# Performance work log

Hardware: AMD Instinct MI355X
Metric: run time of the kernel (lower is better)

The kernel has to match this reference:

```python
import jax, jax.numpy as jnp
import numpy as np

B, T, D = 32, 1024, 512

def _xavier(key, shape):
    fan_in, fan_out = shape[1], shape[0]
    bound = float(np.sqrt(6.0 / (fan_in + fan_out)))
    return jax.random.uniform(key, shape, jnp.float32, -bound, bound)

def setup_inputs() -> dict:
    key = jax.random.key(0)
    ks = jax.random.split(key, 10)
    lin_bound = float(1.0 / np.sqrt(D))
    def lin(kw, kb):
        W = jax.random.uniform(kw, (D, D), jnp.float32, -lin_bound, lin_bound)
        b = jax.random.uniform(kb, (D,), jnp.float32, -lin_bound, lin_bound)
        return W, b
    Wk_w, Wk_b = lin(ks[0], ks[1])
    Wv_w, Wv_b = lin(ks[2], ks[3])
    Wq_w, Wq_b = lin(ks[4], ks[5])
    Wo_w, Wo_b = lin(ks[6], ks[7])
    w = _xavier(ks[8], (T, T))
    x = jax.random.normal(ks[9], (B, T, D), jnp.float32)
    return {"x": x, "Wk_w": Wk_w, "Wk_b": Wk_b, "Wv_w": Wv_w, "Wv_b": Wv_b,
            "Wq_w": Wq_w, "Wq_b": Wq_b, "w": w, "Wo_w": Wo_w, "Wo_b": Wo_b}

def reference(x, Wk_w, Wk_b, Wv_w, Wv_b, Wq_w, Wq_b, w, Wo_w, Wo_b):
    # K, V, Q: [B, T, D]  (torch Linear: x @ W.T + b)
    K = jnp.einsum('btd,ed->bte', x, Wk_w) + Wk_b
    V = jnp.einsum('btd,ed->bte', x, Wv_w) + Wv_b
    # exp_w: [T, T], row-wise max-stabilized position bias
    exp_w = jnp.exp(w - jnp.max(w, axis=-1, keepdims=True))
    # Faithful to original: max over dim=0 (batch dim) of K
    exp_K = jnp.exp(K - jnp.max(K, axis=0, keepdims=True))  # [B, T, D]
    num = jnp.einsum('ts,bsd->btd', exp_w, exp_K * V)
    den = jnp.einsum('ts,bsd->btd', exp_w, exp_K)
    Yt = num / den
    Q = jnp.einsum('btd,ed->bte', x, Wq_w) + Wq_b
    Yt = jax.nn.sigmoid(Q) * Yt
    out = jnp.einsum('btd,ed->bte', Yt, Wo_w) + Wo_b
    return out
```

## Files before the change

kernel.cpp:

```cpp
#include <hip/hip_runtime.h>
#include <stdint.h>

typedef unsigned short u16;
typedef __attribute__((ext_vector_type(4))) float f32x4;
typedef __attribute__((ext_vector_type(8))) __bf16 bf16x8;

__device__ __forceinline__ float b2f(u16 u) {
  union { unsigned int i; float f; } v; v.i = ((unsigned int)u) << 16; return v.f;
}
__device__ __forceinline__ u16 f2b(float f) {
  union { float f; unsigned int i; } v; v.f = f;
  unsigned int x = v.i;
  return (u16)((x + 0x7fffu + ((x >> 16) & 1u)) >> 16);
}

__device__ __forceinline__ void async_ld16(const u16* g, u16* l) {
  __builtin_amdgcn_global_load_lds((const __attribute__((address_space(1))) void*)g,
                                   (__attribute__((address_space(3))) void*)l, 16, 0, 0);
}

__global__ void detect_kernel(const u16* __restrict__ x, int* __restrict__ flag)
{
  const int tid = threadIdx.x;
  int found = 0;
  for (int i = tid; i < 32768; i += 256) {
    u16 u = x[i];
    if ((u & 0x7F80u) == 0x7F80u) found = 1;
  }
  unsigned long long m = __ballot(found != 0);
  __shared__ int sf[4];
  if ((tid & 63) == 0) sf[tid >> 6] = (m != 0ULL) ? 1 : 0;
  __syncthreads();
  if (tid == 0) flag[0] = (sf[0] | sf[1] | sf[2] | sf[3]);
}

__global__ __launch_bounds__(256)
void conv_kernel(const void* __restrict__ in, u16* __restrict__ out, long n,
                 const int* __restrict__ flag)
{
  const long i = ((long)blockIdx.x * 256 + threadIdx.x) * 8;
  if (i >= n) return;
  if (flag[0]) {
    const float* p = (const float*)in + i;
    u16 o[8];
#pragma unroll
    for (int j = 0; j < 8; j++) o[j] = f2b(p[j]);
    *(uint4*)(out + i) = *(const uint4*)o;
  } else {
    *(uint4*)(out + i) = *(const uint4*)((const u16*)in + i);
  }
}

__global__ __launch_bounds__(256)
void conv4_kernel(const void* __restrict__ i0, const void* __restrict__ i1,
                  const void* __restrict__ i2, const void* __restrict__ i3,
                  u16* __restrict__ o0, u16* __restrict__ o1,
                  u16* __restrict__ o2, u16* __restrict__ o3,
                  const int* __restrict__ flag)
{
  const int sel = blockIdx.x >> 7;
  const int blk = blockIdx.x & 127;
  const void* in = (sel == 0) ? i0 : (sel == 1) ? i1 : (sel == 2) ? i2 : i3;
  u16* out = (sel == 0) ? o0 : (sel == 1) ? o1 : (sel == 2) ? o2 : o3;
  const long i = ((long)blk * 256 + threadIdx.x) * 8;
  if (flag[0]) {
    const float* p = (const float*)in + i;
    u16 o[8];
#pragma unroll
    for (int j = 0; j < 8; j++) o[j] = f2b(p[j]);
    *(uint4*)(out + i) = *(const uint4*)o;
  } else {
    *(uint4*)(out + i) = *(const uint4*)((const u16*)in + i);
  }
}

#define BM 128
#define BN 128
#define BK 32

template<int EPI>
__global__ __launch_bounds__(256)
void gemm_bt(const u16* __restrict__ A, const u16* __restrict__ B,
             const void* __restrict__ bias, void* __restrict__ Cv,
             const int* __restrict__ flag,
             int M, int N, int K, long strideC)
{
  __shared__ __align__(16) u16 sA[2][BM * BK];
  __shared__ __align__(16) u16 sB[2][BN * BK];

  const int tid  = threadIdx.x;
  const int lane = tid & 63;
  const int wv   = tid >> 6;
  const int fl = flag[0];
  u16* Cb16 = (u16*)Cv;

  int bx = blockIdx.x, by = blockIdx.y;
  {
    const int nx = gridDim.x, ny = gridDim.y;
    if ((nx & 7) == 0) {
      const int d   = bx + nx * by;
      const int xcd = d & 7;
      const int s   = d >> 3;
      const int q   = s / ny;
      bx = xcd * (nx >> 3) + q;
      by = s - q * ny;
    }
  }
  const int m0 = bx * BM;
  const int n0 = by * BN;

  const int ldRow = wv * 32;
  const int lr = lane >> 2;
  const int lc = lane & 3;
  const int scol = (lc ^ ((lr >> 1) & 3)) * 8;
  const u16* gA = A + (long)(m0 + ldRow + lr) * K + scol;
  const u16* gB = B + (long)(n0 + ldRow + lr) * K + scol;
  const int off0 = (ldRow + lr) * BK + lc * 8;
  const int off1 = (ldRow + 16 + lr) * BK + lc * 8;

  f32x4 acc[4][4];
#pragma unroll
  for (int i = 0; i < 4; i++)
#pragma unroll
    for (int j = 0; j < 4; j++) acc[i][j] = (f32x4)0.0f;

  const int waveM = (wv >> 1) * 64;
  const int waveN = (wv & 1) * 64;
  const int quad  = lane >> 4;
  const int ll    = lane & 15;
  const int rs    = (quad ^ ((ll >> 1) & 3)) * 8;

  async_ld16(gA,          sA[0] + off0);
  async_ld16(gA + 16 * K, sA[0] + off1);
  async_ld16(gB,          sB[0] + off0);
  async_ld16(gB + 16 * K, sB[0] + off1);
  gA += BK; gB += BK;

  const int NT = K / BK;
  for (int t = 0; t < NT; ++t) {
    __syncthreads();
    const int cur = t & 1;
    if (t + 1 < NT) {
      u16* dA = sA[cur ^ 1];
      u16* dB = sB[cur ^ 1];
      async_ld16(gA,          dA + off0);
      async_ld16(gA + 16 * K, dA + off1);
      async_ld16(gB,          dB + off0);
      async_ld16(gB + 16 * K, dB + off1);
      gA += BK; gB += BK;
    }
    const u16* rA = sA[cur];
    const u16* rB = sB[cur];
    bf16x8 aF[4], bF[4];
#pragma unroll
    for (int i = 0; i < 4; i++) {
      aF[i] = *(const bf16x8*)(rA + (waveM + i * 16 + ll) * BK + rs);
      bF[i] = *(const bf16x8*)(rB + (waveN + i * 16 + ll) * BK + rs);
    }
#pragma unroll
    for (int i = 0; i < 4; i++)
#pragma unroll
      for (int j = 0; j < 4; j++)
        acc[i][j] = __builtin_amdgcn_mfma_f32_16x16x32_bf16(aF[i], bF[j], acc[i][j], 0, 0, 0);
  }

#pragma unroll
  for (int i = 0; i < 4; i++) {
    const int rowb = m0 + waveM + i * 16 + quad * 4;
#pragma unroll
    for (int j = 0; j < 4; j++) {
      const int col = n0 + waveN + j * 16 + ll;
      const float bv = fl ? ((const float*)bias)[col] : b2f(((const u16*)bias)[col]);
#pragma unroll
      for (int r = 0; r < 4; r++) {
        const long idx = (long)(rowb + r) * N + col;
        const float v = acc[i][j][r] + bv;
        if (EPI == 0) {
          Cb16[idx] = f2b(v);
        } else {
          const long g = strideC + idx;
          if (fl) ((float*)Cv)[g] = v;
          else    ((u16*)Cv)[g]   = f2b(v);
        }
      }
    }
  }
}

__global__ __launch_bounds__(256)
void gemm_proj3(const u16* __restrict__ A, const u16* __restrict__ Bw,
                const void* __restrict__ kb, const void* __restrict__ vb,
                const void* __restrict__ qb,
                u16* __restrict__ Kp, u16* __restrict__ Vp, u16* __restrict__ Qp,
                const int* __restrict__ flag, int M)
{
  const int KD = 512;
  __shared__ __align__(16) u16 sA[2][BM * BK];
  __shared__ __align__(16) u16 sB[2][BN * BK];

  const int tid  = threadIdx.x;
  const int lane = tid & 63;
  const int wv   = tid >> 6;
  const int fl = flag[0];

  int bx = blockIdx.x, by = blockIdx.y;
  {
    const int nx = gridDim.x, ny = gridDim.y;
    if ((nx & 7) == 0) {
      const int d   = bx + nx * by;
      const int xcd = d & 7;
      const int s   = d >> 3;
      const int q   = s / ny;
      bx = xcd * (nx >> 3) + q;
      by = s - q * ny;
    }
  }
  const int m0 = bx * BM;
  const int n0 = by * BN;

  const int ldRow = wv * 32;
  const int lr = lane >> 2;
  const int lc = lane & 3;
  const int scol = (lc ^ ((lr >> 1) & 3)) * 8;
  const u16* gA = A  + (long)(m0 + ldRow + lr) * KD + scol;
  const u16* gB = Bw + (long)(n0 + ldRow + lr) * KD + scol;
  const int off0 = (ldRow + lr) * BK + lc * 8;
  const int off1 = (ldRow + 16 + lr) * BK + lc * 8;

  f32x4 acc[4][4];
#pragma unroll
  for (int i = 0; i < 4; i++)
#pragma unroll
    for (int j = 0; j < 4; j++) acc[i][j] = (f32x4)0.0f;

  const int waveM = (wv >> 1) * 64;
  const int waveN = (wv & 1) * 64;
  const int quad  = lane >> 4;
  const int ll    = lane & 15;
  const int rs    = (quad ^ ((ll >> 1) & 3)) * 8;

  async_ld16(gA,           sA[0] + off0);
  async_ld16(gA + 16 * KD, sA[0] + off1);
  async_ld16(gB,           sB[0] + off0);
  async_ld16(gB + 16 * KD, sB[0] + off1);
  gA += BK; gB += BK;

  const int NT = KD / BK;
  for (int t = 0; t < NT; ++t) {
    __syncthreads();
    const int cur = t & 1;
    if (t + 1 < NT) {
      u16* dA = sA[cur ^ 1];
      u16* dB = sB[cur ^ 1];
      async_ld16(gA,           dA + off0);
      async_ld16(gA + 16 * KD, dA + off1);
      async_ld16(gB,           dB + off0);
      async_ld16(gB + 16 * KD, dB + off1);
      gA += BK; gB += BK;
    }
    const u16* rA = sA[cur];
    const u16* rB = sB[cur];
    bf16x8 aF[4], bF[4];
#pragma unroll
    for (int i = 0; i < 4; i++) {
      aF[i] = *(const bf16x8*)(rA + (waveM + i * 16 + ll) * BK + rs);
      bF[i] = *(const bf16x8*)(rB + (waveN + i * 16 + ll) * BK + rs);
    }
#pragma unroll
    for (int i = 0; i < 4; i++)
#pragma unroll
      for (int j = 0; j < 4; j++)
        acc[i][j] = __builtin_amdgcn_mfma_f32_16x16x32_bf16(aF[i], bF[j], acc[i][j], 0, 0, 0);
  }

#pragma unroll
  for (int i = 0; i < 4; i++) {
    const int rowb = m0 + waveM + i * 16 + quad * 4;
#pragma unroll
    for (int j = 0; j < 4; j++) {
      const int col = n0 + waveN + j * 16 + ll;
      const int sel = col >> 9;
      const int cs  = col & 511;
      const void* bp = (sel == 0) ? kb : (sel == 1) ? vb : qb;
      u16* dst = (sel == 0) ? Kp : (sel == 1) ? Vp : Qp;
      const float bv = fl ? ((const float*)bp)[cs] : b2f(((const u16*)bp)[cs]);
#pragma unroll
      for (int r = 0; r < 4; r++)
        dst[(long)(rowb + r) * 512 + cs] = f2b(acc[i][j][r] + bv);
    }
  }
}

#define AM 128
#define AN 64
#define ABK 32

__global__ __launch_bounds__(256, 2)
void gemm_aft(const u16* __restrict__ ew, const u16* __restrict__ Pt,
              const u16* __restrict__ PVt, const u16* __restrict__ Q,
              u16* __restrict__ Yt)
{
  const int T = 1024, D = 512;
  __shared__ __align__(16) u16 sA[2][AM * ABK];
  __shared__ __align__(16) u16 sB[2][AN * ABK];
  __shared__ __align__(16) u16 sC[2][AN * ABK];

  const int tid  = threadIdx.x;
  const int lane = tid & 63;
  const int wv   = tid >> 6;

  int xt = blockIdx.x, yt = blockIdx.y, zt = blockIdx.z;
  {
    const int nz = gridDim.z;
    const int d   = xt + (yt << 3) + (zt << 6);
    const int xcd = d & 7;
    const int s   = d >> 3;
    const int panel = xcd * nz + (s >> 3);
    xt = s & 7;
    yt = panel & 7;
    zt = panel >> 3;
  }
  const int b = zt;

  const u16* Ptb  = Pt  + (long)b * D * T;
  const u16* PVtb = PVt + (long)b * D * T;
  const u16* Qb   = Q   + (long)b * T * D;
  u16*       Ytb  = Yt  + (long)b * T * D;

  const int m0 = xt * AM;
  const int n0 = yt * AN;

  const int ldRow = wv * 16;
  const int lr = lane >> 2;
  const int lc = lane & 3;
  const int scol = (lc ^ ((lr >> 1) & 3)) * 8;
  const u16* gA = ew   + (long)(m0 + ldRow + lr) * T + scol;
  const u16* gB = Ptb  + (long)(n0 + ldRow + lr) * T + scol;
  const u16* gC = PVtb + (long)(n0 + ldRow + lr) * T + scol;
  const int offA0 = (ldRow + lr) * ABK + lc * 8;
  const int offA1 = (64 + ldRow + lr) * ABK + lc * 8;
  const int offB0 = (ldRow + lr) * ABK + lc * 8;

  f32x4 accN[4][2], accD[4][2];
#pragma unroll
  for (int i = 0; i < 4; i++)
#pragma unroll
    for (int j = 0; j < 2; j++) { accN[i][j] = (f32x4)0.0f; accD[i][j] = (f32x4)0.0f; }

  const int waveM = (wv >> 1) * 64;
  const int waveN = (wv & 1) * 32;
  const int quad  = lane >> 4;
  const int ll    = lane & 15;
  const int rs    = (quad ^ ((ll >> 1) & 3)) * 8;

  async_ld16(gA,          sA[0] + offA0);
  async_ld16(gA + 64 * T, sA[0] + offA1);
  async_ld16(gB,          sB[0] + offB0);
  async_ld16(gC,          sC[0] + offB0);
  gA += ABK; gB += ABK; gC += ABK;

  const int NT = T / ABK;
  for (int t = 0; t < NT; ++t) {
    __syncthreads();
    const int cur = t & 1;
    if (t + 1 < NT) {
      u16* dA = sA[cur ^ 1];
      u16* dB = sB[cur ^ 1];
      u16* dC = sC[cur ^ 1];
      async_ld16(gA,          dA + offA0);
      async_ld16(gA + 64 * T, dA + offA1);
      async_ld16(gB,          dB + offB0);
      async_ld16(gC,          dC + offB0);
      gA += ABK; gB += ABK; gC += ABK;
    }
    const u16* rA = sA[cur];
    const u16* rB = sB[cur];
    const u16* rC = sC[cur];
    bf16x8 aF[4], bF[2], cF[2];
#pragma unroll
    for (int i = 0; i < 4; i++)
      aF[i] = *(const bf16x8*)(rA + (waveM + i * 16 + ll) * ABK + rs);
#pragma unroll
    for (int j = 0; j < 2; j++) {
      bF[j] = *(const bf16x8*)(rB + (waveN + j * 16 + ll) * ABK + rs);
      cF[j] = *(const bf16x8*)(rC + (waveN + j * 16 + ll) * ABK + rs);
    }
#pragma unroll
    for (int i = 0; i < 4; i++)
#pragma unroll
      for (int j = 0; j < 2; j++) {
        accD[i][j] = __builtin_amdgcn_mfma_f32_16x16x32_bf16(aF[i], bF[j], accD[i][j], 0, 0, 0);
        accN[i][j] = __builtin_amdgcn_mfma_f32_16x16x32_bf16(aF[i], cF[j], accN[i][j], 0, 0, 0);
      }
  }

#pragma unroll
  for (int i = 0; i < 4; i++) {
    const int rowb = m0 + waveM + i * 16 + quad * 4;
#pragma unroll
    for (int j = 0; j < 2; j++) {
      const int col = n0 + waveN + j * 16 + ll;
#pragma unroll
      for (int r = 0; r < 4; r++) {
        const long idx = (long)(rowb + r) * D + col;
        const float q  = b2f(Qb[idx]);
        const float t  = __expf(-q);
        const float rc = __builtin_amdgcn_rcpf(accD[i][j][r] * (1.0f + t));
        Ytb[idx] = f2b(accN[i][j][r] * rc);
      }
    }
  }
}

__global__ __launch_bounds__(256)
void expw_kernel(const void* __restrict__ w, u16* __restrict__ ew,
                 const int* __restrict__ flag)
{
  const int fl = flag[0];
  const int t = blockIdx.x;
  const int tid = threadIdx.x;
  float v[4];
  float m = -1e30f;
#pragma unroll
  for (int i = 0; i < 4; i++) {
    const long idx = (long)t * 1024 + tid + i * 256;
    float val = fl ? ((const float*)w)[idx] : b2f(((const u16*)w)[idx]);
    v[i] = val; m = fmaxf(m, val);
  }
#pragma unroll
  for (int off = 32; off > 0; off >>= 1) m = fmaxf(m, __shfl_xor(m, off, 64));
  __shared__ float sm[4];
  if ((tid & 63) == 0) sm[tid >> 6] = m;
  __syncthreads();
  m = fmaxf(fmaxf(sm[0], sm[1]), fmaxf(sm[2], sm[3]));
  u16* orow = ew + (long)t * 1024;
#pragma unroll
  for (int i = 0; i < 4; i++) orow[tid + i * 256] = f2b(__expf(v[i] - m));
}

__global__ __launch_bounds__(256)
void kmax_kernel(const u16* __restrict__ K, u16* __restrict__ Km)
{
  const long TD = 1024L * 512;
  const long base = ((long)blockIdx.x * 256 + threadIdx.x) * 8;
  float m[8];
#pragma unroll
  for (int j = 0; j < 8; j++) m[j] = -1e30f;
  for (int b = 0; b < 32; b++) {
    uint4 u = *(const uint4*)(K + b * TD + base);
    const u16* p = (const u16*)&u;
#pragma unroll
    for (int j = 0; j < 8; j++) m[j] = fmaxf(m[j], b2f(p[j]));
  }
  u16 outv[8];
#pragma unroll
  for (int j = 0; j < 8; j++) outv[j] = f2b(m[j]);
  *(uint4*)(Km + base) = *(const uint4*)outv;
}

__global__ __launch_bounds__(256)
void pexp_kernel(const u16* __restrict__ K, const u16* __restrict__ V,
                 const u16* __restrict__ Km,
                 u16* __restrict__ Pt, u16* __restrict__ PVt)
{
  const int T = 1024, D = 512;
  const long TD = (long)T * D;
  const int s0 = blockIdx.x * 64;
  const int d0 = blockIdx.y * 64;
  const int b  = blockIdx.z;
  __shared__ u16 lp[64 * 66];
  __shared__ u16 lpv[64 * 66];
  const int tid  = threadIdx.x;
  const int srow = tid >> 3;
  const int c8   = (tid & 7) * 8;

#pragma unroll
  for (int h = 0; h < 2; h++) {
    const int s = srow + h * 32;
    const long gidx = (long)b * TD + (long)(s0 + s) * D + d0 + c8;
    uint4 ku = *(const uint4*)(K + gidx);
    uint4 vu = *(const uint4*)(V + gidx);
    uint4 mu = *(const uint4*)(Km + (long)(s0 + s) * D + d0 + c8);
    const u16* kp = (const u16*)&ku;
    const u16* vp = (const u16*)&vu;
    const u16* mp = (const u16*)&mu;
#pragma unroll
    for (int j = 0; j < 8; j++) {
      float p  = __expf(b2f(kp[j]) - b2f(mp[j]));
      float pv = p * b2f(vp[j]);
      lp[s * 66 + c8 + j]  = f2b(p);
      lpv[s * 66 + c8 + j] = f2b(pv);
    }
  }
  __syncthreads();

  const int lane = tid & 63;
  const int wv   = tid >> 6;
#pragma unroll
  for (int it = 0; it < 16; it++) {
    const int d = wv * 16 + it;
    const long oidx = (long)b * TD + (long)(d0 + d) * T + s0 + lane;
    Pt[oidx]  = lp[lane * 66 + d];
    PVt[oidx] = lpv[lane * 66 + d];
  }
}

extern "C" void kernel_launch(void* const* d_in, const int* in_sizes, int n_in,
                              void* d_out, int out_size, void* d_ws, size_t ws_size,
                              hipStream_t stream)
{
  const int B = 32, T = 1024, D = 512;
  const long TD = (long)T * D;
  const void* x    = d_in[0];
  const void* Wk_w = d_in[1];
  const void* Wk_b = d_in[2];
  const void* Wv_w = d_in[3];
  const void* Wv_b = d_in[4];
  const void* Wq_w = d_in[5];
  const void* Wq_b = d_in[6];
  const void* w    = d_in[7];
  const void* Wo_w = d_in[8];
  const void* Wo_b = d_in[9];

  char* ws = (char*)d_ws;
  const size_t MB = 1024 * 1024;
  u16* xb    = (u16*)(ws + 0);
  u16* Kbuf  = (u16*)(ws + 32 * MB);
  u16* ewb   = (u16*)(ws + 64 * MB);
  u16* kmb   = (u16*)(ws + 66 * MB);
  u16* Wpack = (u16*)(ws + 67 * MB);
  u16* Wvb   = Wpack + 512 * 512;
  u16* Wqb   = Wpack + 2 * 512 * 512;
  u16* Wob   = (u16*)(ws + 68 * MB + 512 * 1024);
  int* flag  = (int*)(ws + 69 * MB);
  u16* Ytb   = Kbuf;

  dim3 blk(256);

  detect_kernel<<<dim3(1), blk, 0, stream>>>((const u16*)x, flag);
  conv_kernel<<<dim3(8192), blk, 0, stream>>>(x, xb, (long)B * T * D, flag);
  conv4_kernel<<<dim3(512), blk, 0, stream>>>(Wk_w, Wv_w, Wq_w, Wo_w,
                                              Wpack, Wvb, Wqb, Wob, flag);
  expw_kernel<<<dim3(1024), blk, 0, stream>>>(w, ewb, flag);

  if (ws_size >= 200 * MB) {
    u16* Vb   = (u16*)(ws + 70 * MB);
    u16* Qb   = (u16*)(ws + 102 * MB);
    u16* Ptb  = (u16*)(ws + 134 * MB);
    u16* PVtb = (u16*)(ws + 166 * MB);

    gemm_proj3<<<dim3((B * T) / 128, 12), blk, 0, stream>>>(
        xb, Wpack, Wk_b, Wv_b, Wq_b, Kbuf, Vb, Qb, flag, B * T);

    kmax_kernel<<<dim3(256), blk, 0, stream>>>(Kbuf, kmb);
    pexp_kernel<<<dim3(16, 8, 32), blk, 0, stream>>>(Kbuf, Vb, kmb, Ptb, PVtb);

    gemm_aft<<<dim3(T / AM, D / AN, 32), blk, 0, stream>>>(ewb, Ptb, PVtb, Qb, Ytb);

    gemm_bt<3><<<dim3((B * T) / 128, D / 128), blk, 0, stream>>>(
        Ytb, Wob, Wo_b, d_out, flag, B * T, D, D, 0);
  } else {
    const int NB = 4, NC = B / NB;
    char* ck = ws + 70 * MB;
    const size_t cb = (size_t)NB * TD * sizeof(u16);
    u16* Vc   = (u16*)(ck);
    u16* Ptc  = (u16*)(ck + cb);
    u16* PVtc = (u16*)(ck + 2 * cb);
    u16* Qc   = (u16*)(ck + 3 * cb);
    u16* Ytc  = Vc;

    gemm_bt<0><<<dim3((B * T) / 128, D / 128), blk, 0, stream>>>(
        xb, Wpack, Wk_b, Kbuf, flag, B * T, D, D, 0);
    kmax_kernel<<<dim3(256), blk, 0, stream>>>(Kbuf, kmb);

    dim3 gP((NB * T) / 128, D / 128, 1);
    dim3 gA(T / AM, D / AN, NB);
    for (int c = 0; c < NC; c++) {
      const long off = (long)c * NB * TD;
      gemm_bt<0><<<gP, blk, 0, stream>>>(xb + off, Wvb, Wv_b, Vc, flag, NB * T, D, D, 0);
      gemm_bt<0><<<gP, blk, 0, stream>>>(xb + off, Wqb, Wq_b, Qc, flag, NB * T, D, D, 0);
      pexp_kernel<<<dim3(16, 8, NB), blk, 0, stream>>>(Kbuf + off, Vc, kmb, Ptc, PVtc);
      gemm_aft<<<gA, blk, 0, stream>>>(ewb, Ptc, PVtc, Qc, Ytc);
      gemm_bt<3><<<gP, blk, 0, stream>>>(Ytc, Wob, Wo_b, d_out, flag, NB * T, D, D, off);
    }
  }
}
```

Before: 379.6 us.

## Triple-buffer LDS tiles with partial vmcnt waits in all GEMM kernels

Moves the three GEMM kernels (generic, fused QKV projection, AFT num/den) from double- to triple-buffered shared-memory staging. Loads now run two K-tiles ahead, and the full __syncthreads is replaced by an s_waitcnt vmcnt(4) plus barrier, so only the oldest tile's loads must land before compute. This is meant to hide more global-load latency behind MFMA work. In exchange it uses 50% more LDS per block, which may reduce occupancy, and the correctness of the hand-written wait counts depends on each thread issuing exactly four loads per tile.

```diff
diff --git a/kernel.cpp b/kernel.cpp
--- a/kernel.cpp
+++ b/kernel.cpp
@@ -17,6 +17,17 @@
 __device__ __forceinline__ void async_ld16(const u16* g, u16* l) {
   __builtin_amdgcn_global_load_lds((const __attribute__((address_space(1))) void*)g,
                                    (__attribute__((address_space(3))) void*)l, 16, 0, 0);
+}
+
+__device__ __forceinline__ void pipe_wait4() {
+  asm volatile("s_waitcnt vmcnt(4)" ::: "memory");
+  __builtin_amdgcn_s_barrier();
+  asm volatile("" ::: "memory");
+}
+__device__ __forceinline__ void pipe_wait0() {
+  asm volatile("s_waitcnt vmcnt(0)" ::: "memory");
+  __builtin_amdgcn_s_barrier();
+  asm volatile("" ::: "memory");
 }
 
 __global__ void detect_kernel(const u16* __restrict__ x, int* __restrict__ flag)
@@ -85,8 +96,8 @@
              const int* __restrict__ flag,
              int M, int N, int K, long strideC)
 {
-  __shared__ __align__(16) u16 sA[2][BM * BK];
-  __shared__ __align__(16) u16 sB[2][BN * BK];
+  __shared__ __align__(16) u16 sA[3][BM * BK];
+  __shared__ __align__(16) u16 sB[3][BN * BK];
 
   const int tid  = threadIdx.x;
   const int lane = tid & 63;
@@ -135,14 +146,20 @@
   async_ld16(gB,          sB[0] + off0);
   async_ld16(gB + 16 * K, sB[0] + off1);
   gA += BK; gB += BK;
+  async_ld16(gA,          sA[1] + off0);
+  async_ld16(gA + 16 * K, sA[1] + off1);
+  async_ld16(gB,          sB[1] + off0);
+  async_ld16(gB + 16 * K, sB[1] + off1);
+  gA += BK; gB += BK;
 
   const int NT = K / BK;
+  int cur = 0;
   for (int t = 0; t < NT; ++t) {
-    __syncthreads();
-    const int cur = t & 1;
-    if (t + 1 < NT) {
-      u16* dA = sA[cur ^ 1];
-      u16* dB = sB[cur ^ 1];
+    if (t < NT - 1) pipe_wait4(); else pipe_wait0();
+    if (t + 2 < NT) {
+      int pre = cur + 2; if (pre >= 3) pre -= 3;
+      u16* dA = sA[pre];
+      u16* dB = sB[pre];
       async_ld16(gA,          dA + off0);
       async_ld16(gA + 16 * K, dA + off1);
       async_ld16(gB,          dB + off0);
@@ -162,6 +179,7 @@
 #pragma unroll
       for (int j = 0; j < 4; j++)
         acc[i][j] = __builtin_amdgcn_mfma_f32_16x16x32_bf16(aF[i], bF[j], acc[i][j], 0, 0, 0);
+    cur += 1; if (cur == 3) cur = 0;
   }
 
 #pragma unroll
@@ -195,8 +213,8 @@
                 const int* __restrict__ flag, int M)
 {
   const int KD = 512;
-  __shared__ __align__(16) u16 sA[2][BM * BK];
-  __shared__ __align__(16) u16 sB[2][BN * BK];
+  __shared__ __align__(16) u16 sA[3][BM * BK];
+  __shared__ __align__(16) u16 sB[3][BN * BK];
 
   const int tid  = threadIdx.x;
   const int lane = tid & 63;
@@ -244,14 +262,20 @@
   async_ld16(gB,           sB[0] + off0);
   async_ld16(gB + 16 * KD, sB[0] + off1);
   gA += BK; gB += BK;
+  async_ld16(gA,           sA[1] + off0);
+  async_ld16(gA + 16 * KD, sA[1] + off1);
+  async_ld16(gB,           sB[1] + off0);
+  async_ld16(gB + 16 * KD, sB[1] + off1);
+  gA += BK; gB += BK;
 
   const int NT = KD / BK;
+  int cur = 0;
   for (int t = 0; t < NT; ++t) {
-    __syncthreads();
-    const int cur = t & 1;
-    if (t + 1 < NT) {
-      u16* dA = sA[cur ^ 1];
-      u16* dB = sB[cur ^ 1];
+    if (t < NT - 1) pipe_wait4(); else pipe_wait0();
+    if (t + 2 < NT) {
+      int pre = cur + 2; if (pre >= 3) pre -= 3;
+      u16* dA = sA[pre];
+      u16* dB = sB[pre];
       async_ld16(gA,           dA + off0);
       async_ld16(gA + 16 * KD, dA + off1);
       async_ld16(gB,           dB + off0);
@@ -271,6 +295,7 @@
 #pragma unroll
       for (int j = 0; j < 4; j++)
         acc[i][j] = __builtin_amdgcn_mfma_f32_16x16x32_bf16(aF[i], bF[j], acc[i][j], 0, 0, 0);
+    cur += 1; if (cur == 3) cur = 0;
   }
 
 #pragma unroll
@@ -301,9 +326,9 @@
               u16* __restrict__ Yt)
 {
   const int T = 1024, D = 512;
-  __shared__ __align__(16) u16 sA[2][AM * ABK];
-  __shared__ __align__(16) u16 sB[2][AN * ABK];
-  __shared__ __align__(16) u16 sC[2][AN * ABK];
+  __shared__ __align__(16) u16 sA[3][AM * ABK];
+  __shared__ __align__(16) u16 sB[3][AN * ABK];
+  __shared__ __align__(16) u16 sC[3][AN * ABK];
 
   const int tid  = threadIdx.x;
   const int lane = tid & 63;
@@ -358,15 +383,21 @@
   async_ld16(gB,          sB[0] + offB0);
   async_ld16(gC,          sC[0] + offB0);
   gA += ABK; gB += ABK; gC += ABK;
+  async_ld16(gA,          sA[1] + offA0);
+  async_ld16(gA + 64 * T, sA[1] + offA1);
+  async_ld16(gB,          sB[1] + offB0);
+  async_ld16(gC,          sC[1] + offB0);
+  gA += ABK; gB += ABK; gC += ABK;
 
   const int NT = T / ABK;
+  int cur = 0;
   for (int t = 0; t < NT; ++t) {
-    __syncthreads();
-    const int cur = t & 1;
-    if (t + 1 < NT) {
-      u16* dA = sA[cur ^ 1];
-      u16* dB = sB[cur ^ 1];
-      u16* dC = sC[cur ^ 1];
+    if (t < NT - 1) pipe_wait4(); else pipe_wait0();
+    if (t + 2 < NT) {
+      int pre = cur + 2; if (pre >= 3) pre -= 3;
+      u16* dA = sA[pre];
+      u16* dB = sB[pre];
+      u16* dC = sC[pre];
       async_ld16(gA,          dA + offA0);
       async_ld16(gA + 64 * T, dA + offA1);
       async_ld16(gB,          dB + offB0);
@@ -392,6 +423,7 @@
         accD[i][j] = __builtin_amdgcn_mfma_f32_16x16x32_bf16(aF[i], bF[j], accD[i][j], 0, 0, 0);
         accN[i][j] = __builtin_amdgcn_mfma_f32_16x16x32_bf16(aF[i], cF[j], accN[i][j], 0, 0, 0);
       }
+    cur += 1; if (cur == 3) cur = 0;
   }
 
 #pragma unroll
```

New measurement: 383.0 us. No clear change (+0.9%).

## Enlarge AFT GEMM tile to 256x128 with 8 waves and interleaved prefetch

Applied to the files above, without the earlier changes.

Rewrites gemm_aft to use 512-thread blocks, each computing a 256x128 output tile with a K step of 64 split into two 32-wide sub-stages. Global-to-LDS prefetch of the next stage is interleaved between MFMA phases, with explicit barriers, waitcnt and setprio to overlap memory and compute. The XCD-aware block remapping is adjusted to the new 4x4 grid. Larger tiles cut redundant loads of exp_w and P tiles. In exchange the kernel uses more LDS and registers, which may lower occupancy, and the hand-written waitcnt sequence is fragile.

```diff
diff --git a/kernel.cpp b/kernel.cpp
--- a/kernel.cpp
+++ b/kernel.cpp
@@ -291,19 +291,15 @@
   }
 }
 
-#define AM 128
-#define AN 64
-#define ABK 32
-
-__global__ __launch_bounds__(256, 2)
+__global__ __launch_bounds__(512, 2)
 void gemm_aft(const u16* __restrict__ ew, const u16* __restrict__ Pt,
               const u16* __restrict__ PVt, const u16* __restrict__ Q,
               u16* __restrict__ Yt)
 {
   const int T = 1024, D = 512;
-  __shared__ __align__(16) u16 sA[2][AM * ABK];
-  __shared__ __align__(16) u16 sB[2][AN * ABK];
-  __shared__ __align__(16) u16 sC[2][AN * ABK];
+  __shared__ __align__(16) u16 sA[2 * 2 * 256 * 32];
+  __shared__ __align__(16) u16 sB[2 * 2 * 128 * 32];
+  __shared__ __align__(16) u16 sC[2 * 2 * 128 * 32];
 
   const int tid  = threadIdx.x;
   const int lane = tid & 63;
@@ -312,79 +308,85 @@
   int xt = blockIdx.x, yt = blockIdx.y, zt = blockIdx.z;
   {
     const int nz = gridDim.z;
-    const int d   = xt + (yt << 3) + (zt << 6);
-    const int xcd = d & 7;
-    const int s   = d >> 3;
-    const int panel = xcd * nz + (s >> 3);
-    xt = s & 7;
-    yt = panel & 7;
-    zt = panel >> 3;
+    if ((nz & 1) == 0) {
+      const int d   = xt + (yt << 2) + (zt << 4);
+      const int xcd = d & 7;
+      const int s   = d >> 3;
+      xt = s & 3;
+      const int p = xcd * (nz >> 1) + (s >> 2);
+      yt = p & 3;
+      zt = p >> 2;
+    }
   }
   const int b = zt;
-
   const u16* Ptb  = Pt  + (long)b * D * T;
   const u16* PVtb = PVt + (long)b * D * T;
   const u16* Qb   = Q   + (long)b * T * D;
   u16*       Ytb  = Yt  + (long)b * T * D;
-
-  const int m0 = xt * AM;
-  const int n0 = yt * AN;
-
-  const int ldRow = wv * 16;
-  const int lr = lane >> 2;
-  const int lc = lane & 3;
-  const int scol = (lc ^ ((lr >> 1) & 3)) * 8;
-  const u16* gA = ew   + (long)(m0 + ldRow + lr) * T + scol;
-  const u16* gB = Ptb  + (long)(n0 + ldRow + lr) * T + scol;
-  const u16* gC = PVtb + (long)(n0 + ldRow + lr) * T + scol;
-  const int offA0 = (ldRow + lr) * ABK + lc * 8;
-  const int offA1 = (64 + ldRow + lr) * ABK + lc * 8;
-  const int offB0 = (ldRow + lr) * ABK + lc * 8;
-
-  f32x4 accN[4][2], accD[4][2];
-#pragma unroll
-  for (int i = 0; i < 4; i++)
+  const int m0 = xt * 256;
+  const int n0 = yt * 128;
+
+  const int sr = tid >> 2, ss = tid & 3;
+  const int sslot = (ss ^ ((sr >> 1) & 3)) * 8;
+  const u16* gA0 = ew   + (long)(m0 + sr)       * T + sslot;
+  const u16* gA1 = ew   + (long)(m0 + 128 + sr) * T + sslot;
+  const u16* gB  = Ptb  + (long)(n0 + sr)       * T + sslot;
+  const u16* gC  = PVtb + (long)(n0 + sr)       * T + sslot;
+  const int soff = sr * 32 + ss * 8;
+
+  f32x4 accN[8][2], accD[8][2];
+#pragma unroll
+  for (int i = 0; i < 8; i++)
 #pragma unroll
     for (int j = 0; j < 2; j++) { accN[i][j] = (f32x4)0.0f; accD[i][j] = (f32x4)0.0f; }
 
-  const int waveM = (wv >> 1) * 64;
-  const int waveN = (wv & 1) * 32;
   const int quad  = lane >> 4;
   const int ll    = lane & 15;
   const int rs    = (quad ^ ((ll >> 1) & 3)) * 8;
-
-  async_ld16(gA,          sA[0] + offA0);
-  async_ld16(gA + 64 * T, sA[0] + offA1);
-  async_ld16(gB,          sB[0] + offB0);
-  async_ld16(gC,          sC[0] + offB0);
-  gA += ABK; gB += ABK; gC += ABK;
-
-  const int NT = T / ABK;
+  const int waveM = (wv >> 2) * 128;
+  const int waveN = (wv & 3) * 32;
+
+  async_ld16(gA0,      sA + soff);
+  async_ld16(gA1,      sA + 4096 + soff);
+  async_ld16(gB,       sB + soff);
+  async_ld16(gC,       sC + soff);
+  async_ld16(gA0 + 32, sA + 8192 + soff);
+  async_ld16(gA1 + 32, sA + 8192 + 4096 + soff);
+  async_ld16(gB  + 32, sB + 4096 + soff);
+  async_ld16(gC  + 32, sC + 4096 + soff);
+  asm volatile("s_waitcnt vmcnt(4)" ::: "memory");
+  __builtin_amdgcn_s_barrier();
+
+  const int NT = T / 64;
   for (int t = 0; t < NT; ++t) {
-    __syncthreads();
     const int cur = t & 1;
-    if (t + 1 < NT) {
-      u16* dA = sA[cur ^ 1];
-      u16* dB = sB[cur ^ 1];
-      u16* dC = sC[cur ^ 1];
-      async_ld16(gA,          dA + offA0);
-      async_ld16(gA + 64 * T, dA + offA1);
-      async_ld16(gB,          dB + offB0);
-      async_ld16(gC,          dC + offB0);
-      gA += ABK; gB += ABK; gC += ABK;
-    }
-    const u16* rA = sA[cur];
-    const u16* rB = sB[cur];
-    const u16* rC = sC[cur];
+    const u16* bA = sA + cur * 16384;
+    const u16* bB = sB + cur * 8192;
+    const u16* bC = sC + cur * 8192;
+    u16* nA = sA + (cur ^ 1) * 16384;
+    u16* nB = sB + (cur ^ 1) * 8192;
+    u16* nC = sC + (cur ^ 1) * 8192;
+    const int ko = (t + 1) * 64;
+    const bool st = (t + 1 < NT);
+
     bf16x8 aF[4], bF[2], cF[2];
-#pragma unroll
-    for (int i = 0; i < 4; i++)
-      aF[i] = *(const bf16x8*)(rA + (waveM + i * 16 + ll) * ABK + rs);
+
+#pragma unroll
+    for (int i = 0; i < 4; i++)
+      aF[i] = *(const bf16x8*)(bA + (waveM + i * 16 + ll) * 32 + rs);
 #pragma unroll
     for (int j = 0; j < 2; j++) {
-      bF[j] = *(const bf16x8*)(rB + (waveN + j * 16 + ll) * ABK + rs);
-      cF[j] = *(const bf16x8*)(rC + (waveN + j * 16 + ll) * ABK + rs);
-    }
+      bF[j] = *(const bf16x8*)(bB + (waveN + j * 16 + ll) * 32 + rs);
+      cF[j] = *(const bf16x8*)(bC + (waveN + j * 16 + ll) * 32 + rs);
+    }
+    if (st) {
+      async_ld16(gA0 + ko, nA + soff);
+      async_ld16(gA1 + ko, nA + 4096 + soff);
+    }
+    __builtin_amdgcn_s_barrier();
+    asm volatile("s_waitcnt lgkmcnt(0)" ::: "memory");
+    __builtin_amdgcn_sched_barrier(0);
+    __builtin_amdgcn_s_setprio(1);
 #pragma unroll
     for (int i = 0; i < 4; i++)
 #pragma unroll
@@ -392,10 +394,87 @@
         accD[i][j] = __builtin_amdgcn_mfma_f32_16x16x32_bf16(aF[i], bF[j], accD[i][j], 0, 0, 0);
         accN[i][j] = __builtin_amdgcn_mfma_f32_16x16x32_bf16(aF[i], cF[j], accN[i][j], 0, 0, 0);
       }
-  }
-
-#pragma unroll
-  for (int i = 0; i < 4; i++) {
+    __builtin_amdgcn_s_setprio(0);
+    __builtin_amdgcn_s_barrier();
+
+#pragma unroll
+    for (int i = 0; i < 4; i++)
+      aF[i] = *(const bf16x8*)(bA + (waveM + (4 + i) * 16 + ll) * 32 + rs);
+    if (st) {
+      async_ld16(gB + ko, nB + soff);
+      async_ld16(gC + ko, nC + soff);
+    }
+    __builtin_amdgcn_s_barrier();
+    asm volatile("s_waitcnt lgkmcnt(0)" ::: "memory");
+    __builtin_amdgcn_sched_barrier(0);
+    __builtin_amdgcn_s_setprio(1);
+#pragma unroll
+    for (int i = 0; i < 4; i++)
+#pragma unroll
+      for (int j = 0; j < 2; j++) {
+        accD[4 + i][j] = __builtin_amdgcn_mfma_f32_16x16x32_bf16(aF[i], bF[j], accD[4 + i][j], 0, 0, 0);
+        accN[4 + i][j] = __builtin_amdgcn_mfma_f32_16x16x32_bf16(aF[i], cF[j], accN[4 + i][j], 0, 0, 0);
+      }
+    __builtin_amdgcn_s_setprio(0);
+    if (st) asm volatile("s_waitcnt vmcnt(4)" ::: "memory");
+    else    asm volatile("s_waitcnt vmcnt(0)" ::: "memory");
+    __builtin_amdgcn_s_barrier();
+
+    const u16* bA1 = bA + 8192;
+    const u16* bB1 = bB + 4096;
+    const u16* bC1 = bC + 4096;
+#pragma unroll
+    for (int i = 0; i < 4; i++)
+      aF[i] = *(const bf16x8*)(bA1 + (waveM + i * 16 + ll) * 32 + rs);
+#pragma unroll
+    for (int j = 0; j < 2; j++) {
+      bF[j] = *(const bf16x8*)(bB1 + (waveN + j * 16 + ll) * 32 + rs);
+      cF[j] = *(const bf16x8*)(bC1 + (waveN + j * 16 + ll) * 32 + rs);
+    }
+    if (st) {
+      async_ld16(gA0 + ko + 32, nA + 8192 + soff);
+      async_ld16(gA1 + ko + 32, nA + 8192 + 4096 + soff);
+    }
+    __builtin_amdgcn_s_barrier();
+    asm volatile("s_waitcnt lgkmcnt(0)" ::: "memory");
+    __builtin_amdgcn_sched_barrier(0);
+    __builtin_amdgcn_s_setprio(1);
+#pragma unroll
+    for (int i = 0; i < 4; i++)
+#pragma unroll
+      for (int j = 0; j < 2; j++) {
+        accD[i][j] = __builtin_amdgcn_mfma_f32_16x16x32_bf16(aF[i], bF[j], accD[i][j], 0, 0, 0);
+        accN[i][j] = __builtin_amdgcn_mfma_f32_16x16x32_bf16(aF[i], cF[j], accN[i][j], 0, 0, 0);
+      }
+    __builtin_amdgcn_s_setprio(0);
+    __builtin_amdgcn_s_barrier();
+
+#pragma unroll
+    for (int i = 0; i < 4; i++)
+      aF[i] = *(const bf16x8*)(bA1 + (waveM + (4 + i) * 16 + ll) * 32 + rs);
+    if (st) {
+      async_ld16(gB + ko + 32, nB + 4096 + soff);
+      async_ld16(gC + ko + 32, nC + 4096 + soff);
+    }
+    __builtin_amdgcn_s_barrier();
+    asm volatile("s_waitcnt lgkmcnt(0)" ::: "memory");
+    __builtin_amdgcn_sched_barrier(0);
+    __builtin_amdgcn_s_setprio(1);
+#pragma unroll
+    for (int i = 0; i < 4; i++)
+#pragma unroll
+      for (int j = 0; j < 2; j++) {
+        accD[4 + i][j] = __builtin_amdgcn_mfma_f32_16x16x32_bf16(aF[i], bF[j], accD[4 + i][j], 0, 0, 0);
+        accN[4 + i][j] = __builtin_amdgcn_mfma_f32_16x16x32_bf16(aF[i], cF[j], accN[4 + i][j], 0, 0, 0);
+      }
+    __builtin_amdgcn_s_setprio(0);
+    if (st) asm volatile("s_waitcnt vmcnt(4)" ::: "memory");
+    else    asm volatile("s_waitcnt vmcnt(0)" ::: "memory");
+    __builtin_amdgcn_s_barrier();
+  }
+
+#pragma unroll
+  for (int i = 0; i < 8; i++) {
     const int rowb = m0 + waveM + i * 16 + quad * 4;
 #pragma unroll
     for (int j = 0; j < 2; j++) {
@@ -404,8 +483,8 @@
       for (int r = 0; r < 4; r++) {
         const long idx = (long)(rowb + r) * D + col;
         const float q  = b2f(Qb[idx]);
-        const float t  = __expf(-q);
-        const float rc = __builtin_amdgcn_rcpf(accD[i][j][r] * (1.0f + t));
+        const float e  = __expf(-q);
+        const float rc = __builtin_amdgcn_rcpf(accD[i][j][r] * (1.0f + e));
         Ytb[idx] = f2b(accN[i][j][r] * rc);
       }
     }
@@ -555,7 +634,7 @@
     kmax_kernel<<<dim3(256), blk, 0, stream>>>(Kbuf, kmb);
     pexp_kernel<<<dim3(16, 8, 32), blk, 0, stream>>>(Kbuf, Vb, kmb, Ptb, PVtb);
 
-    gemm_aft<<<dim3(T / AM, D / AN, 32), blk, 0, stream>>>(ewb, Ptb, PVtb, Qb, Ytb);
+    gemm_aft<<<dim3(4, 4, 32), dim3(512), 0, stream>>>(ewb, Ptb, PVtb, Qb, Ytb);
 
     gemm_bt<3><<<dim3((B * T) / 128, D / 128), blk, 0, stream>>>(
         Ytb, Wob, Wo_b, d_out, flag, B * T, D, D, 0);
@@ -574,13 +653,13 @@
     kmax_kernel<<<dim3(256), blk, 0, stream>>>(Kbuf, kmb);
 
     dim3 gP((NB * T) / 128, D / 128, 1);
-    dim3 gA(T / AM, D / AN, NB);
+    dim3 gA(4, 4, NB);
     for (int c = 0; c < NC; c++) {
       const long off = (long)c * NB * TD;
       gemm_bt<0><<<gP, blk, 0, stream>>>(xb + off, Wvb, Wv_b, Vc, flag, NB * T, D, D, 0);
       gemm_bt<0><<<gP, blk, 0, stream>>>(xb + off, Wqb, Wq_b, Qc, flag, NB * T, D, D, 0);
       pexp_kernel<<<dim3(16, 8, NB), blk, 0, stream>>>(Kbuf + off, Vc, kmb, Ptc, PVtc);
-      gemm_aft<<<gA, blk, 0, stream>>>(ewb, Ptc, PVtc, Qc, Ytc);
+      gemm_aft<<<gA, dim3(512), 0, stream>>>(ewb, Ptc, PVtc, Qc, Ytc);
       gemm_bt<3><<<gP, blk, 0, stream>>>(Ytc, Wob, Wo_b, d_out, flag, NB * T, D, D, off);
     }
   }
```

Result: no change. 378.2 us (-0.4%).
